# Kernel optimization log

Measured on AMD Instinct MI355X. Metric: run time of the kernel, lower is better.

The kernel has to match this reference:

```python
import jax, jax.numpy as jnp
import numpy as np

EMB_DIM = 1024
HEAD_SIZE = 64
SEQ = 2048
BATCH = 8


def setup_inputs() -> dict:
    key = jax.random.key(0)
    kx, kq, kk, kv = jax.random.split(key, 4)
    x = jax.random.normal(kx, (BATCH, SEQ, EMB_DIM), dtype=jnp.float32)
    # nn.Linear(E, H, bias=False): y = x @ W.T with W of shape [H, E]; store as [E, H]
    s = 1.0 / np.sqrt(EMB_DIM)
    Wq = jax.random.uniform(kq, (EMB_DIM, HEAD_SIZE), jnp.float32, -s, s)
    Wk = jax.random.uniform(kk, (EMB_DIM, HEAD_SIZE), jnp.float32, -s, s)
    Wv = jax.random.uniform(kv, (EMB_DIM, HEAD_SIZE), jnp.float32, -s, s)
    return {"x": x, "Wq": Wq, "Wk": Wk, "Wv": Wv}


def reference(x, Wq, Wk, Wv):
    B, S, E = x.shape
    q = jnp.einsum("bse,eh->bsh", x, Wq)
    k = jnp.einsum("bse,eh->bsh", x, Wk)
    v = jnp.einsum("bse,eh->bsh", x, Wv)
    # NOTE: original scales by E**-0.5 (embedding dim), not head_size**-0.5
    att = jnp.einsum("bqh,bkh->bqk", q, k) * (E ** -0.5)
    causal = jnp.tril(jnp.ones((S, S), dtype=bool))
    att = jnp.where(causal, att, -jnp.inf)
    att = jax.nn.softmax(att, axis=-1)
    # dropout(p=0.2) treated as identity (eval mode) for deterministic reference
    out = jnp.einsum("bqk,bkh->bqh", att, v)
    return out
```

## Files before the change

### kernel.cpp

```cpp
#include <hip/hip_runtime.h>

constexpr int Bn = 8, S = 2048, E = 1024, H = 64;
constexpr float SCALE = 0.03125f;
constexpr float LOG2E = 1.44269504f;

typedef __attribute__((ext_vector_type(8))) short short8;
typedef __attribute__((ext_vector_type(4))) float f32x4;

__device__ __forceinline__ unsigned short f2bf(float f) {
  unsigned u = __builtin_bit_cast(unsigned, f);
  u += 0x7fffu + ((u >> 16) & 1u);
  return (unsigned short)(u >> 16);
}
__device__ __forceinline__ ushort4 f4bf(float4 f) {
  return make_ushort4(f2bf(f.x), f2bf(f.y), f2bf(f.z), f2bf(f.w));
}

__global__ __launch_bounds__(256) void wtrans_kernel(
    const float* __restrict__ Wq, const float* __restrict__ Wk,
    const float* __restrict__ Wv, unsigned short* __restrict__ WT3) {
  __shared__ unsigned short tb[64][72];
  const int m = blockIdx.x >> 4;
  const int e0 = (blockIdx.x & 15) * 64;
  const float* W = (m == 0) ? Wq : (m == 1) ? Wk : Wv;
  const int t = threadIdx.x;
#pragma unroll
  for (int it = 0; it < 4; ++it) {
    int idx = t + it * 256;
    int r = idx >> 4, c4 = idx & 15;
    float4 f = ((const float4*)(W + (long)(e0 + r) * H))[c4];
    *(ushort4*)&tb[r][c4 * 4] = f4bf(f);
  }
  __syncthreads();
#pragma unroll
  for (int it = 0; it < 4; ++it) {
    int idx = t + it * 256;
    int h = idx >> 4, e4 = idx & 15;
    ushort4 u = make_ushort4(tb[e4 * 4 + 0][h], tb[e4 * 4 + 1][h],
                             tb[e4 * 4 + 2][h], tb[e4 * 4 + 3][h]);
    ((ushort4*)(WT3 + (long)(m * 64 + h) * E + e0))[e4] = u;
  }
}

__global__ __launch_bounds__(256, 4) void qkv_kernel(
    const float* __restrict__ x, const unsigned short* __restrict__ WT3,
    unsigned short* __restrict__ q, unsigned short* __restrict__ kk,
    unsigned short* __restrict__ vT) {
  __shared__ unsigned short xs[16][72];
  const int t = threadIdx.x;
  const int w = t >> 6, lane = t & 63, l15 = lane & 15, g = lane >> 4;
  const long row0 = (long)blockIdx.x * 16;
  const int xr = t >> 4, xc = t & 15;

  f32x4 acc[3];
#pragma unroll
  for (int ct = 0; ct < 3; ++ct) acc[ct] = f32x4{0.f, 0.f, 0.f, 0.f};

  float4 px = ((const float4*)(x + (row0 + xr) * E))[xc];
  *(ushort4*)&xs[xr][xc * 4] = f4bf(px);
  const unsigned short* wbase = WT3 + (long)(w * 48 + l15) * E + g * 8;

  for (int c = 0; c < 16; ++c) {
    __syncthreads();
    if (c < 15)
      px = ((const float4*)(x + (row0 + xr) * E + (c + 1) * 64))[xc];
    short8 a0 = *(const short8*)&xs[l15][g * 8];
    short8 a1 = *(const short8*)&xs[l15][32 + g * 8];
#pragma unroll
    for (int ct = 0; ct < 3; ++ct) {
      short8 b0 = *(const short8*)(wbase + (long)(ct * 16) * E + c * 64);
      short8 b1 = *(const short8*)(wbase + (long)(ct * 16) * E + c * 64 + 32);
      acc[ct] = __builtin_amdgcn_mfma_f32_16x16x32_bf16(a0, b0, acc[ct], 0, 0, 0);
      acc[ct] = __builtin_amdgcn_mfma_f32_16x16x32_bf16(a1, b1, acc[ct], 0, 0, 0);
    }
    __syncthreads();
    if (c < 15) *(ushort4*)&xs[xr][xc * 4] = f4bf(px);
  }

  const int bb = (int)(row0 >> 11);
  const int srow = (int)(row0 & 2047);
#pragma unroll
  for (int ct = 0; ct < 3; ++ct) {
    const int col = w * 48 + ct * 16 + l15;
    const int mm = col >> 6, ch = col & 63;
    if (mm == 0) {
#pragma unroll
      for (int r = 0; r < 4; ++r)
        q[(row0 + g * 4 + r) * H + ch] = f2bf(acc[ct][r] * SCALE);
    } else if (mm == 1) {
#pragma unroll
      for (int r = 0; r < 4; ++r)
        kk[(row0 + g * 4 + r) * H + ch] = f2bf(acc[ct][r]);
    } else {
      ushort4 v4 = make_ushort4(f2bf(acc[ct][0]), f2bf(acc[ct][1]),
                                f2bf(acc[ct][2]), f2bf(acc[ct][3]));
      *(ushort4*)(vT + ((long)bb * H + ch) * S + srow + g * 4) = v4;
    }
  }
}

__global__ __launch_bounds__(256, 2) void attn_kernel(
    const unsigned short* __restrict__ q, const unsigned short* __restrict__ k,
    const unsigned short* __restrict__ vT, float* __restrict__ out) {
  __shared__ unsigned short pl[4][16][72];
  __shared__ float Om[2][64][20];
  __shared__ float ms[2][16], ls[2][16];
  const int t = threadIdx.x;
  const int w = t >> 6, lane = t & 63, l15 = lane & 15, g = lane >> 4;
  const int b = blockIdx.x & 7, p = blockIdx.x >> 3;
  const int grp = w >> 1, sp = w & 1;
  const int qt = grp ? (127 - p) : p;
  const int qrow0 = qt * 16;
  const int nt = (16 * qt + 79) >> 6;
  const unsigned short* kb = k + (long)b * S * H;
  const unsigned short* vb = vT + (long)b * H * S;
  const unsigned short* qp = q + ((long)b * S + qrow0 + l15) * H + g * 8;
  short8 bq0 = *(const short8*)qp;
  short8 bq1 = *(const short8*)(qp + 32);

  f32x4 O[4];
#pragma unroll
  for (int c = 0; c < 4; ++c) O[c] = f32x4{0.f, 0.f, 0.f, 0.f};
  float m_ = -1e30f, l_ = 0.f;

  short8 ak[4][2];
  int kt = sp;
  if (kt < nt) {
#pragma unroll
    for (int c = 0; c < 4; ++c)
#pragma unroll
      for (int kh = 0; kh < 2; ++kh)
        ak[c][kh] = *(const short8*)(kb + (long)(kt * 64 + c * 16 + l15) * H + kh * 32 + g * 8);
  }

  for (; kt < nt; kt += 2) {
    short8 av[4][2];
#pragma unroll
    for (int c = 0; c < 4; ++c)
#pragma unroll
      for (int kh = 0; kh < 2; ++kh)
        av[c][kh] = *(const short8*)(vb + (long)(c * 16 + l15) * S + kt * 64 + kh * 32 + g * 8);
    f32x4 sc[4];
#pragma unroll
    for (int c = 0; c < 4; ++c) {
      sc[c] = f32x4{0.f, 0.f, 0.f, 0.f};
      sc[c] = __builtin_amdgcn_mfma_f32_16x16x32_bf16(ak[c][0], bq0, sc[c], 0, 0, 0);
      sc[c] = __builtin_amdgcn_mfma_f32_16x16x32_bf16(ak[c][1], bq1, sc[c], 0, 0, 0);
    }
    if (kt + 2 < nt) {
#pragma unroll
      for (int c = 0; c < 4; ++c)
#pragma unroll
        for (int kh = 0; kh < 2; ++kh)
          ak[c][kh] = *(const short8*)(kb + (long)((kt + 2) * 64 + c * 16 + l15) * H + kh * 32 + g * 8);
    }
    if (kt == nt - 1) {
#pragma unroll
      for (int c = 0; c < 4; ++c)
#pragma unroll
        for (int r = 0; r < 4; ++r)
          if (kt * 64 + c * 16 + g * 4 + r > qrow0 + l15) sc[c][r] = -1e30f;
    }
    float mx = -1e30f;
#pragma unroll
    for (int c = 0; c < 4; ++c)
#pragma unroll
      for (int r = 0; r < 4; ++r) mx = fmaxf(mx, sc[c][r]);
    mx = fmaxf(mx, __shfl_xor(mx, 16));
    mx = fmaxf(mx, __shfl_xor(mx, 32));
    float mn = fmaxf(m_, mx);
    float al = exp2f((m_ - mn) * LOG2E);
    float sum = 0.f;
#pragma unroll
    for (int c = 0; c < 4; ++c)
#pragma unroll
      for (int r = 0; r < 4; ++r) {
        float pe = exp2f((sc[c][r] - mn) * LOG2E);
        sc[c][r] = pe;
        sum += pe;
      }
    sum += __shfl_xor(sum, 16);
    sum += __shfl_xor(sum, 32);
    l_ = l_ * al + sum;
    m_ = mn;
#pragma unroll
    for (int c = 0; c < 4; ++c) {
      ushort4 p4 = make_ushort4(f2bf(sc[c][0]), f2bf(sc[c][1]),
                                f2bf(sc[c][2]), f2bf(sc[c][3]));
      *(ushort4*)&pl[w][l15][c * 16 + g * 4] = p4;
    }
#pragma unroll
    for (int c = 0; c < 4; ++c)
#pragma unroll
      for (int r = 0; r < 4; ++r) O[c][r] *= al;
    short8 bp0 = *(const short8*)&pl[w][l15][g * 8];
    short8 bp1 = *(const short8*)&pl[w][l15][32 + g * 8];
#pragma unroll
    for (int c = 0; c < 4; ++c) {
      O[c] = __builtin_amdgcn_mfma_f32_16x16x32_bf16(av[c][0], bp0, O[c], 0, 0, 0);
      O[c] = __builtin_amdgcn_mfma_f32_16x16x32_bf16(av[c][1], bp1, O[c], 0, 0, 0);
    }
  }

  if (sp == 1) {
#pragma unroll
    for (int c = 0; c < 4; ++c)
#pragma unroll
      for (int r = 0; r < 4; ++r)
        Om[grp][c * 16 + g * 4 + r][l15] = O[c][r];
    if (g == 0) { ms[grp][l15] = m_; ls[grp][l15] = l_; }
  }
  __syncthreads();
  if (sp == 0) {
    float m1 = ms[grp][l15], l1 = ls[grp][l15];
    float mstar = fmaxf(m_, m1);
    float f0 = exp2f((m_ - mstar) * LOG2E);
    float f1 = exp2f((m1 - mstar) * LOG2E);
    float inv = 1.0f / (l_ * f0 + l1 * f1);
    float* op = out + ((long)b * S + qrow0 + l15) * H;
#pragma unroll
    for (int c = 0; c < 4; ++c) {
      float4 o;
      o.x = (O[c][0] * f0 + Om[grp][c * 16 + g * 4 + 0][l15] * f1) * inv;
      o.y = (O[c][1] * f0 + Om[grp][c * 16 + g * 4 + 1][l15] * f1) * inv;
      o.z = (O[c][2] * f0 + Om[grp][c * 16 + g * 4 + 2][l15] * f1) * inv;
      o.w = (O[c][3] * f0 + Om[grp][c * 16 + g * 4 + 3][l15] * f1) * inv;
      *(float4*)(op + c * 16 + g * 4) = o;
    }
  }
}

extern "C" void kernel_launch(void* const* d_in, const int* in_sizes, int n_in,
                              void* d_out, int out_size, void* d_ws, size_t ws_size,
                              hipStream_t stream) {
  const float* x  = (const float*)d_in[0];
  const float* Wq = (const float*)d_in[1];
  const float* Wk = (const float*)d_in[2];
  const float* Wv = (const float*)d_in[3];
  float* outp = (float*)d_out;
  unsigned short* WT3 = (unsigned short*)d_ws;
  unsigned short* q  = (unsigned short*)((char*)d_ws + 512 * 1024);
  unsigned short* kk = q + (size_t)Bn * S * H;
  unsigned short* vT = kk + (size_t)Bn * S * H;
  wtrans_kernel<<<dim3(48), dim3(256), 0, stream>>>(Wq, Wk, Wv, WT3);
  qkv_kernel<<<dim3((Bn * S) / 16), dim3(256), 0, stream>>>(x, WT3, q, kk, vT);
  attn_kernel<<<dim3(Bn * 64), dim3(256), 0, stream>>>(q, kk, vT, outp);
}
```

Baseline: 172.9 us.

## Stage weight tiles in LDS and double rows per block in QKV projection

The QKV projection kernel now processes 32 rows per block instead of 16 and stages both the x tile and the 192x128 bf16 weight slice in shared memory, with a 128-wide K step. Each weight fragment loaded from LDS feeds two MFMAs, one per row tile, which halves global weight traffic per output row and removes the per-wave strided global weight loads. The cost is much larger LDS use (about 60KB), more prefetch registers and a dropped occupancy hint, so fewer blocks fit per CU and the grid has half as many blocks.

```diff
diff --git a/kernel.cpp b/kernel.cpp
--- a/kernel.cpp
+++ b/kernel.cpp
@@ -42,39 +42,70 @@
   }
 }
 
-__global__ __launch_bounds__(256, 4) void qkv_kernel(
+__global__ __launch_bounds__(256) void qkv_kernel(
     const float* __restrict__ x, const unsigned short* __restrict__ WT3,
     unsigned short* __restrict__ q, unsigned short* __restrict__ kk,
     unsigned short* __restrict__ vT) {
-  __shared__ unsigned short xs[16][72];
+  __shared__ unsigned short xs[32][136];
+  __shared__ unsigned short ws[192][136];
   const int t = threadIdx.x;
   const int w = t >> 6, lane = t & 63, l15 = lane & 15, g = lane >> 4;
-  const long row0 = (long)blockIdx.x * 16;
-  const int xr = t >> 4, xc = t & 15;
-
-  f32x4 acc[3];
-#pragma unroll
-  for (int ct = 0; ct < 3; ++ct) acc[ct] = f32x4{0.f, 0.f, 0.f, 0.f};
-
-  float4 px = ((const float4*)(x + (row0 + xr) * E))[xc];
-  *(ushort4*)&xs[xr][xc * 4] = f4bf(px);
-  const unsigned short* wbase = WT3 + (long)(w * 48 + l15) * E + g * 8;
-
-  for (int c = 0; c < 16; ++c) {
+  const long row0 = (long)blockIdx.x * 32;
+  const int xrow = t >> 5, xslot = t & 31;
+  const int wrow = t >> 4, wslot = t & 15;
+
+  f32x4 acc[2][3];
+#pragma unroll
+  for (int rt = 0; rt < 2; ++rt)
+#pragma unroll
+    for (int ct = 0; ct < 3; ++ct) acc[rt][ct] = f32x4{0.f, 0.f, 0.f, 0.f};
+
+  float4 px[4];
+  short8 pw[12];
+#pragma unroll
+  for (int it = 0; it < 4; ++it)
+    px[it] = ((const float4*)(x + (row0 + xrow + it * 8) * E))[xslot];
+#pragma unroll
+  for (int it = 0; it < 12; ++it)
+    pw[it] = *(const short8*)(WT3 + (long)(wrow + it * 16) * E + wslot * 8);
+#pragma unroll
+  for (int it = 0; it < 4; ++it)
+    *(ushort4*)&xs[xrow + it * 8][xslot * 4] = f4bf(px[it]);
+#pragma unroll
+  for (int it = 0; it < 12; ++it)
+    *(short8*)&ws[wrow + it * 16][wslot * 8] = pw[it];
+
+  for (int c = 0; c < 8; ++c) {
     __syncthreads();
-    if (c < 15)
-      px = ((const float4*)(x + (row0 + xr) * E + (c + 1) * 64))[xc];
-    short8 a0 = *(const short8*)&xs[l15][g * 8];
-    short8 a1 = *(const short8*)&xs[l15][32 + g * 8];
-#pragma unroll
-    for (int ct = 0; ct < 3; ++ct) {
-      short8 b0 = *(const short8*)(wbase + (long)(ct * 16) * E + c * 64);
-      short8 b1 = *(const short8*)(wbase + (long)(ct * 16) * E + c * 64 + 32);
-      acc[ct] = __builtin_amdgcn_mfma_f32_16x16x32_bf16(a0, b0, acc[ct], 0, 0, 0);
-      acc[ct] = __builtin_amdgcn_mfma_f32_16x16x32_bf16(a1, b1, acc[ct], 0, 0, 0);
+    if (c < 7) {
+      const int e0 = (c + 1) * 128;
+#pragma unroll
+      for (int it = 0; it < 4; ++it)
+        px[it] = ((const float4*)(x + (row0 + xrow + it * 8) * E + e0))[xslot];
+#pragma unroll
+      for (int it = 0; it < 12; ++it)
+        pw[it] = *(const short8*)(WT3 + (long)(wrow + it * 16) * E + e0 + wslot * 8);
+    }
+#pragma unroll
+    for (int kh = 0; kh < 4; ++kh) {
+      short8 a0 = *(const short8*)&xs[l15][kh * 32 + g * 8];
+      short8 a1 = *(const short8*)&xs[16 + l15][kh * 32 + g * 8];
+#pragma unroll
+      for (int ct = 0; ct < 3; ++ct) {
+        short8 b = *(const short8*)&ws[w * 48 + ct * 16 + l15][kh * 32 + g * 8];
+        acc[0][ct] = __builtin_amdgcn_mfma_f32_16x16x32_bf16(a0, b, acc[0][ct], 0, 0, 0);
+        acc[1][ct] = __builtin_amdgcn_mfma_f32_16x16x32_bf16(a1, b, acc[1][ct], 0, 0, 0);
+      }
     }
     __syncthreads();
-    if (c < 15) *(ushort4*)&xs[xr][xc * 4] = f4bf(px);
+    if (c < 7) {
+#pragma unroll
+      for (int it = 0; it < 4; ++it)
+        *(ushort4*)&xs[xrow + it * 8][xslot * 4] = f4bf(px[it]);
+#pragma unroll
+      for (int it = 0; it < 12; ++it)
+        *(short8*)&ws[wrow + it * 16][wslot * 8] = pw[it];
+    }
   }
 
   const int bb = (int)(row0 >> 11);
@@ -83,18 +114,22 @@
   for (int ct = 0; ct < 3; ++ct) {
     const int col = w * 48 + ct * 16 + l15;
     const int mm = col >> 6, ch = col & 63;
-    if (mm == 0) {
-#pragma unroll
-      for (int r = 0; r < 4; ++r)
-        q[(row0 + g * 4 + r) * H + ch] = f2bf(acc[ct][r] * SCALE);
-    } else if (mm == 1) {
-#pragma unroll
-      for (int r = 0; r < 4; ++r)
-        kk[(row0 + g * 4 + r) * H + ch] = f2bf(acc[ct][r]);
-    } else {
-      ushort4 v4 = make_ushort4(f2bf(acc[ct][0]), f2bf(acc[ct][1]),
-                                f2bf(acc[ct][2]), f2bf(acc[ct][3]));
-      *(ushort4*)(vT + ((long)bb * H + ch) * S + srow + g * 4) = v4;
+#pragma unroll
+    for (int rt = 0; rt < 2; ++rt) {
+      const int srl = rt * 16 + g * 4;
+      if (mm == 0) {
+#pragma unroll
+        for (int r = 0; r < 4; ++r)
+          q[(row0 + srl + r) * H + ch] = f2bf(acc[rt][ct][r] * SCALE);
+      } else if (mm == 1) {
+#pragma unroll
+        for (int r = 0; r < 4; ++r)
+          kk[(row0 + srl + r) * H + ch] = f2bf(acc[rt][ct][r]);
+      } else {
+        ushort4 v4 = make_ushort4(f2bf(acc[rt][ct][0]), f2bf(acc[rt][ct][1]),
+                                  f2bf(acc[rt][ct][2]), f2bf(acc[rt][ct][3]));
+        *(ushort4*)(vT + ((long)bb * H + ch) * S + srow + srl) = v4;
+      }
     }
   }
 }
@@ -243,6 +278,6 @@
   unsigned short* kk = q + (size_t)Bn * S * H;
   unsigned short* vT = kk + (size_t)Bn * S * H;
   wtrans_kernel<<<dim3(48), dim3(256), 0, stream>>>(Wq, Wk, Wv, WT3);
-  qkv_kernel<<<dim3((Bn * S) / 16), dim3(256), 0, stream>>>(x, WT3, q, kk, vT);
+  qkv_kernel<<<dim3((Bn * S) / 32), dim3(256), 0, stream>>>(x, WT3, q, kk, vT);
   attn_kernel<<<dim3(Bn * 64), dim3(256), 0, stream>>>(q, kk, vT, outp);
 }
```

Measured after the change: 141.1 us. -18.4%, faster.
